# Kernel optimization log

Hardware: AMD Instinct MI355X
Metric: run time of the kernel (lower is better)

## Reference

```python
import jax, jax.numpy as jnp
import numpy as np

B, S, H, F, K = 32, 512, 256, 256, 3
NBINS, MAX_MEL = 256, 2048


def _conv1d(x, w, b):
    # x: [B,S,Cin], w: [K,Cin,Cout] -> [B,S,Cout], padding 1 (SAME, k=3)
    return jax.lax.conv_general_dilated(x, w, (1,), 'SAME',
        dimension_numbers=('NWC', 'WIO', 'NWC')) + b


def _ln(x, g, b):
    m = jnp.mean(x, -1, keepdims=True)
    v = jnp.var(x, -1, keepdims=True)
    return (x - m) * jax.lax.rsqrt(v + 1e-5) * g + b


def _predictor(x, mask, p):
    # FastSpeech2 VariancePredictor (eval mode, dropout off)
    w1, b1, g1, be1, w2, b2, g2, be2, wl, bl = p
    h = _ln(jax.nn.relu(_conv1d(x, w1, b1)), g1, be1)
    h = _ln(jax.nn.relu(_conv1d(h, w2, b2)), g2, be2)
    out = (h @ wl + bl)[..., 0]  # [B,S]
    return jnp.where(mask, 0.0, out)  # masked_fill(mask, 0.0)


def _make_predictor_params(key, out_bias):
    ks = jax.random.split(key, 3)
    w1 = jax.random.normal(ks[0], (K, H, F), jnp.float32) * 0.03
    w2 = jax.random.normal(ks[1], (K, F, F), jnp.float32) * 0.03
    wl = jax.random.normal(ks[2], (F, 1), jnp.float32) * 0.02
    return [w1, jnp.zeros((F,), jnp.float32), jnp.ones((F,), jnp.float32), jnp.zeros((F,), jnp.float32),
            w2, jnp.zeros((F,), jnp.float32), jnp.ones((F,), jnp.float32), jnp.zeros((F,), jnp.float32),
            wl, jnp.full((1,), out_bias, jnp.float32)]


PNAMES = ['w1', 'b1', 'g1', 'be1', 'w2', 'b2', 'g2', 'be2', 'wl', 'bl']


def setup_inputs() -> dict:
    key = jax.random.key(0)
    ks = jax.random.split(key, 8)
    inp = {
        'x': jax.random.normal(ks[0], (B, S, H), jnp.float32),
        'src_mask': jnp.zeros((B, S), jnp.bool_),  # True = padded position
        'pitch_control': jnp.float32(1.0),
        'energy_control': jnp.float32(1.0),
        'duration_control': jnp.float32(1.0),
        'pitch_bins': jnp.linspace(-4.0, 4.0, NBINS - 1, dtype=jnp.float32),
        'energy_bins': jnp.linspace(-4.0, 4.0, NBINS - 1, dtype=jnp.float32),
        'pitch_emb': jax.random.normal(ks[1], (NBINS, H), jnp.float32) * 0.02,
        'energy_emb': jax.random.normal(ks[2], (NBINS, H), jnp.float32) * 0.02,
    }
    # duration predictor output bias 1.6 ~ log(5) -> avg ~4 frames/phoneme
    for i, (pref, ob) in enumerate([('dur', 1.6), ('pit', 0.0), ('ene', 0.0)]):
        for n, v in zip(PNAMES, _make_predictor_params(ks[3 + i], ob)):
            inp[pref + '_' + n] = v
    return inp


def reference(x, src_mask, pitch_control, energy_control, duration_control,
              pitch_bins, energy_bins, pitch_emb, energy_emb,
              dur_w1, dur_b1, dur_g1, dur_be1, dur_w2, dur_b2, dur_g2, dur_be2, dur_wl, dur_bl,
              pit_w1, pit_b1, pit_g1, pit_be1, pit_w2, pit_b2, pit_g2, pit_be2, pit_wl, pit_bl,
              ene_w1, ene_b1, ene_g1, ene_be1, ene_w2, ene_b2, ene_g2, ene_be2, ene_wl, ene_bl):
    dur_p = [dur_w1, dur_b1, dur_g1, dur_be1, dur_w2, dur_b2, dur_g2, dur_be2, dur_wl, dur_bl]
    pit_p = [pit_w1, pit_b1, pit_g1, pit_be1, pit_w2, pit_b2, pit_g2, pit_be2, pit_wl, pit_bl]
    ene_p = [ene_w1, ene_b1, ene_g1, ene_be1, ene_w2, ene_b2, ene_g2, ene_be2, ene_wl, ene_bl]

    log_dur = _predictor(x, src_mask, dur_p)                      # [B,S]
    pitch_pred = _predictor(x, src_mask, pit_p) * pitch_control   # inference: scaled prediction
    # torch.bucketize(v, bins) (right=False) == searchsorted side='left'
    x = x + pitch_emb[jnp.searchsorted(pitch_bins, pitch_pred, side='left')]
    energy_pred = _predictor(x, src_mask, ene_p) * energy_control
    x = x + energy_emb[jnp.searchsorted(energy_bins, energy_pred, side='left')]

    dur = jnp.maximum(jnp.round(jnp.exp(log_dur) - 1.0) * duration_control, 0.0)  # [B,S]
    dur_i = dur.astype(jnp.int32)
    mel_len = jnp.minimum(jnp.sum(dur_i, -1), MAX_MEL)            # [B]
    # Length regulator: frame t maps to phoneme idx = #{cumdur <= t}
    cum = jnp.cumsum(dur_i, 1)                                    # [B,S]
    t = jnp.arange(MAX_MEL, dtype=jnp.int32)
    idx = jax.vmap(lambda c: jnp.searchsorted(c, t, side='right'))(cum)  # [B,MAX_MEL]
    idx = jnp.clip(idx, 0, S - 1)
    x_exp = jnp.take_along_axis(x, idx[:, :, None], axis=1)       # [B,MAX_MEL,H]
    mel_mask = t[None, :] >= mel_len[:, None]                     # True = padded frame
    x_exp = jnp.where(mel_mask[:, :, None], 0.0, x_exp)
    return (x_exp, pitch_pred, energy_pred, log_dur, dur, mel_len, mel_mask)
```

## Files before the change

kernel.cpp:

```cpp
#include <hip/hip_runtime.h>
#include <stdint.h>

#define BB 32
#define SS 512
#define HH 256
#define MM (BB*SS)
#define MAXMEL 2048

typedef _Float16 f16;
typedef _Float16 f16x4 __attribute__((ext_vector_type(4)));
typedef _Float16 f16x8 __attribute__((ext_vector_type(8)));
typedef float    f32x16 __attribute__((ext_vector_type(16)));

#define BAR()  asm volatile("s_barrier" ::: "memory")
#define VMW9() asm volatile("s_waitcnt vmcnt(9)" ::: "memory")
#define VMW0() asm volatile("s_waitcnt vmcnt(0)" ::: "memory")

__device__ __forceinline__ size_t xoff8(int pane, int row) {
  return ((size_t)pane * MM + row) * 8;
}

#define AOFF  49152
#define ABUF  12352
#define AZ    61440
#define BBUF  24576
#define LDSSZ 73856
#define WSZP ((size_t)393216)

template<int NS, int RAW>
__global__ __launch_bounds__(256) void conv16(
    const f16* __restrict__ X0h, const f16* __restrict__ X0l,
    const f16* __restrict__ X1h_, const f16* __restrict__ X1l_,
    const f16* __restrict__ W0, const f16* __restrict__ W1,
    const float* __restrict__ bias0, const float* __restrict__ bias1,
    f16* __restrict__ Y0h, f16* __restrict__ Y0l,
    f16* __restrict__ Y1h, f16* __restrict__ Y1l,
    float* __restrict__ Craw)
{
  __shared__ __align__(16) unsigned char smem[LDSSZ];
  const int tid = threadIdx.x;
  const int lane = tid & 63, wid = tid >> 6;
  const int bm = blockIdx.x, bn = blockIdx.y, bz = blockIdx.z;
  const int l31 = lane & 31, half = lane >> 5;
  const int wr = wid >> 1, wc = wid & 1;

  const int s0 = RAW ? bz * 8 : 0;
  const f16* Xh = (RAW || bz == 0) ? X0h : X1h_;
  const f16* Xl = (RAW || bz == 0) ? X0l : X1l_;
  const f16* Wp = (RAW || bz == 0) ? W0 : W1;

  const f16* sb[9]; int sdst[9]; int sdb[9]; size_t sstr[9];
  #pragma unroll
  for (int i = 0; i < 9; ++i) {
    int j = wid * 9 + i;
    if (j < 12) {
      int p = j / 6, rem = j % 6, g = rem / 3, seg = rem % 3;
      int lr = seg * 64 + lane;
      int row = bm * 128 - 32 + lr;
      row = row < 0 ? 0 : (row >= MM ? MM - 1 : row);
      sb[i]   = (p ? Xl : Xh) + ((size_t)g * MM + row) * 8;
      sstr[i] = (size_t)MM * 16;
      sdst[i] = AOFF + p * 6144 + g * 3072 + lr * 16;
      sdb[i]  = ABUF;
    } else {
      int jj = j - 12;
      int p = jj / 12, rest = jj % 12;
      int tap = rest >> 2, q = rest & 3;
      int g = q >> 1, h2 = q & 1;
      sb[i]   = Wp + ((((((size_t)(bn * 16) * 2 + p) * 3 + tap) * 2 + g) * 128)
                      + h2 * 64 + lane) * 8;
      sstr[i] = 12288;
      sdst[i] = p * 12288 + tap * 4096 + g * 2048 + h2 * 1024 + lane * 16;
      sdb[i]  = BBUF;
    }
  }

  int a_addr[3][2][2];
  #pragma unroll
  for (int tap = 0; tap < 3; ++tap)
    #pragma unroll
    for (int mi = 0; mi < 2; ++mi) {
      int row_l = wr * 64 + mi * 32 + l31;
      int sseq = (bm & 3) * 128 + row_l + tap - 1;
      bool valid = (unsigned)sseq < 512u;
      int lr = row_l + tap + 31;
      #pragma unroll
      for (int p = 0; p < 2; ++p)
        a_addr[tap][mi][p] = valid ? (AOFF + p * 6144 + half * 3072 + lr * 16)
                                   : AZ;
    }
  int b_base[2];
  #pragma unroll
  for (int n = 0; n < 2; ++n)
    b_base[n] = half * 2048 + (wc * 64 + n * 32 + l31) * 16;

  f32x16 acc[2][2];
  #pragma unroll
  for (int mi = 0; mi < 2; ++mi)
    #pragma unroll
    for (int ni = 0; ni < 2; ++ni) acc[mi][ni] = (f32x16)0.f;

  auto STAGE = [&](int buf, int step) {
    #pragma unroll
    for (int i = 0; i < 9; ++i)
      __builtin_amdgcn_global_load_lds(
        (const __attribute__((address_space(1))) void*)(sb[i] + (size_t)step * sstr[i]),
        (__attribute__((address_space(3))) void*)(smem + sdst[i] + buf * sdb[i]),
        16, 0, 0);
  };

  auto COMP = [&](int buf) {
    #pragma unroll
    for (int tap = 0; tap < 3; ++tap) {
      f16x8 av[2][2], bv[2][2];
      #pragma unroll
      for (int p = 0; p < 2; ++p)
        #pragma unroll
        for (int q = 0; q < 2; ++q) {
          av[p][q] = *(const f16x8*)(smem + (a_addr[tap][q][p] + buf * ABUF));
          bv[p][q] = *(const f16x8*)(smem + (buf * BBUF + p * 12288 + tap * 4096 + b_base[q]));
        }
      #pragma unroll
      for (int mi = 0; mi < 2; ++mi)
        #pragma unroll
        for (int ni = 0; ni < 2; ++ni) {
          acc[mi][ni] = __builtin_amdgcn_mfma_f32_32x32x16_f16(av[0][mi], bv[0][ni], acc[mi][ni], 0, 0, 0);
          acc[mi][ni] = __builtin_amdgcn_mfma_f32_32x32x16_f16(av[0][mi], bv[1][ni], acc[mi][ni], 0, 0, 0);
          acc[mi][ni] = __builtin_amdgcn_mfma_f32_32x32x16_f16(av[1][mi], bv[0][ni], acc[mi][ni], 0, 0, 0);
        }
    }
  };

  if (tid < 4) {
    *(float4*)(smem + AZ + tid * 16) = make_float4(0.f, 0.f, 0.f, 0.f);
    *(float4*)(smem + AZ + ABUF + tid * 16) = make_float4(0.f, 0.f, 0.f, 0.f);
  }
  STAGE(0, s0); STAGE(1, s0 + 1);
  __syncthreads();

  #pragma unroll
  for (int i = 0; i < NS; ++i) {
    COMP(i & 1);
    BAR();
    if (i < NS - 2)       { STAGE(i & 1, s0 + i + 2); VMW9(); }
    else if (i == NS - 2) { VMW0(); }
    BAR();
  }

  if constexpr (RAW) {
    float* C = Craw + (size_t)bz * MM * 256;
    #pragma unroll
    for (int mi = 0; mi < 2; ++mi)
      #pragma unroll
      for (int ni = 0; ni < 2; ++ni) {
        int colg = bn * 128 + wc * 64 + ni * 32 + l31;
        #pragma unroll
        for (int r = 0; r < 16; ++r) {
          int rowl = (r & 3) + 8 * (r >> 2) + 4 * half;
          size_t rowg = (size_t)bm * 128 + wr * 64 + mi * 32 + rowl;
          C[rowg * 256 + colg] = acc[mi][ni][r];
        }
      }
  } else {
    const float* bias = bz ? bias1 : bias0;
    f16* Yh = bz ? Y1h : Y0h;
    f16* Yl = bz ? Y1l : Y0l;
    #pragma unroll
    for (int mi = 0; mi < 2; ++mi)
      #pragma unroll
      for (int ni = 0; ni < 2; ++ni) {
        int colg = bn * 128 + wc * 64 + ni * 32 + l31;
        float bvs = bias[colg];
        size_t cbase = (size_t)(colg >> 3) * MM * 8 + (colg & 7);
        #pragma unroll
        for (int r = 0; r < 16; ++r) {
          int rowl = (r & 3) + 8 * (r >> 2) + 4 * half;
          int rowg = bm * 128 + wr * 64 + mi * 32 + rowl;
          float v = fmaxf(acc[mi][ni][r] + bvs, 0.f);
          f16 h = (f16)v;
          f16 l = (f16)(v - (float)h);
          size_t o = cbase + (size_t)rowg * 8;
          Yh[o] = h;
          Yl[o] = l;
        }
      }
  }
}

__global__ __launch_bounds__(256) void wsplit6(
    const float* __restrict__ W0, const float* __restrict__ W1,
    const float* __restrict__ W2, const float* __restrict__ W3,
    const float* __restrict__ W4, const float* __restrict__ W5,
    f16* __restrict__ Wt)
{
  int z = blockIdx.y;
  const float* W = z==0?W0 : z==1?W1 : z==2?W2 : z==3?W3 : z==4?W4 : W5;
  f16* T = Wt + (size_t)z * WSZP;
  int id = blockIdx.x * 256 + threadIdx.x;
  int col = id & 127;
  int t = id >> 7;
  int g = t & 1; t >>= 1;
  int tap = t % 3; t /= 3;
  int p = t & 1; t >>= 1;
  int s = t & 15;
  int bn = t >> 4;
  int chan = s * 16 + g * 8;
  int colg = bn * 128 + col;
  f16x8 o;
  #pragma unroll
  for (int e = 0; e < 8; ++e) {
    float w = W[(size_t)(tap * 256 + chan + e) * 256 + colg];
    f16 h = (f16)w;
    o[e] = p ? (f16)(w - (float)h) : h;
  }
  *(f16x8*)(T + (size_t)id * 8) = o;
}

__global__ __launch_bounds__(256) void split2(
    const float* __restrict__ X, f16* __restrict__ Hi, f16* __restrict__ Lo)
{
  int id = blockIdx.x * 256 + threadIdx.x;
  int row = id >> 5, pane = id & 31;
  const float* src = X + (size_t)row * 256 + pane * 8;
  float4 v0 = *(const float4*)src;
  float4 v1 = *(const float4*)(src + 4);
  float vv[8] = {v0.x, v0.y, v0.z, v0.w, v1.x, v1.y, v1.z, v1.w};
  f16x8 h, l;
  #pragma unroll
  for (int j = 0; j < 8; ++j) {
    f16 hh = (f16)vv[j];
    h[j] = hh;
    l[j] = (f16)(vv[j] - (float)hh);
  }
  size_t o = xoff8(pane, row);
  *(f16x8*)(Hi + o) = h;
  *(f16x8*)(Lo + o) = l;
}


__global__ __launch_bounds__(256) void lnF(
    f16* __restrict__ P0h, f16* __restrict__ P0l,
    f16* __restrict__ P1h, f16* __restrict__ P1l,
    const float* __restrict__ g0, const float* __restrict__ be0,
    const float* __restrict__ g1, const float* __restrict__ be1)
{
  int z = blockIdx.y;
  f16* Ph = z ? P1h : P0h;
  f16* Pl = z ? P1l : P0l;
  const float* g  = z ? g1 : g0;
  const float* be = z ? be1 : be0;
  int tid = threadIdx.x, lane = tid & 63;
  int row  = blockIdx.x * 8 + (tid >> 6) * 2 + (lane >> 5);
  int pane = lane & 31;
  size_t o = xoff8(pane, row);
  f16x8 h = *(const f16x8*)(Ph + o);
  f16x8 l = *(const f16x8*)(Pl + o);
  float v[8];
  #pragma unroll
  for (int j = 0; j < 8; ++j) v[j] = (float)h[j] + (float)l[j];
  float s = 0.f, q = 0.f;
  #pragma unroll
  for (int j = 0; j < 8; ++j) { s += v[j]; q += v[j] * v[j]; }
  #pragma unroll
  for (int d = 16; d > 0; d >>= 1) { s += __shfl_xor(s, d); q += __shfl_xor(q, d); }
  float mean = s * (1.f / 256.f);
  float var  = q * (1.f / 256.f) - mean * mean;
  float inv  = 1.0f / sqrtf(var + 1e-5f);
  float4 ga = *(const float4*)(g + pane * 8);
  float4 gb = *(const float4*)(g + pane * 8 + 4);
  float4 ba = *(const float4*)(be + pane * 8);
  float4 bb = *(const float4*)(be + pane * 8 + 4);
  float gv[8] = {ga.x, ga.y, ga.z, ga.w, gb.x, gb.y, gb.z, gb.w};
  float bv[8] = {ba.x, ba.y, ba.z, ba.w, bb.x, bb.y, bb.z, bb.w};
  #pragma unroll
  for (int j = 0; j < 8; ++j) {
    float oo = (v[j] - mean) * inv * gv[j] + bv[j];
    f16 hh = (f16)oo;
    h[j] = hh;
    l[j] = (f16)(oo - (float)hh);
  }
  *(f16x8*)(Ph + o) = h;
  *(f16x8*)(Pl + o) = l;
}

__global__ __launch_bounds__(256) void lnheadD(
    const f16* __restrict__ U0h, const f16* __restrict__ U0l,
    const f16* __restrict__ U1h, const f16* __restrict__ U1l,
    const float* __restrict__ g0, const float* __restrict__ be0,
    const float* __restrict__ wl0, const float* __restrict__ bl0,
    const float* __restrict__ g1, const float* __restrict__ be1,
    const float* __restrict__ wl1, const float* __restrict__ bl1,
    const unsigned char* __restrict__ mask, const float* __restrict__ pc,
    float* __restrict__ o_ldur, float* __restrict__ pred_d,
    float* __restrict__ o_pit,
    const float* __restrict__ pbins, const float* __restrict__ pemb,
    const f16* __restrict__ XPh, const f16* __restrict__ XPl,
    f16* __restrict__ X1h, f16* __restrict__ X1l)
{
  int z = blockIdx.y;
  int tid = threadIdx.x, lane = tid & 63;
  int row  = blockIdx.x * 8 + (tid >> 6) * 2 + (lane >> 5);
  int pane = lane & 31;
  size_t o = xoff8(pane, row);
  const f16* Uh = z ? U1h : U0h;
  const f16* Ul = z ? U1l : U0l;
  f16x8 h = *(const f16x8*)(Uh + o);
  f16x8 l = *(const f16x8*)(Ul + o);
  float v[8];
  #pragma unroll
  for (int j = 0; j < 8; ++j) v[j] = (float)h[j] + (float)l[j];
  float s = 0.f, q = 0.f;
  #pragma unroll
  for (int j = 0; j < 8; ++j) { s += v[j]; q += v[j] * v[j]; }
  #pragma unroll
  for (int d = 16; d > 0; d >>= 1) { s += __shfl_xor(s, d); q += __shfl_xor(q, d); }
  float mean = s * (1.f / 256.f);
  float var  = q * (1.f / 256.f) - mean * mean;
  float inv  = 1.0f / sqrtf(var + 1e-5f);
  const float* g  = z ? g1  : g0;
  const float* be = z ? be1 : be0;
  const float* wl = z ? wl1 : wl0;
  float4 ga = *(const float4*)(g + pane * 8);
  float4 gb = *(const float4*)(g + pane * 8 + 4);
  float4 ba = *(const float4*)(be + pane * 8);
  float4 bb = *(const float4*)(be + pane * 8 + 4);
  float4 wa = *(const float4*)(wl + pane * 8);
  float4 wb = *(const float4*)(wl + pane * 8 + 4);
  float gv[8] = {ga.x, ga.y, ga.z, ga.w, gb.x, gb.y, gb.z, gb.w};
  float bv[8] = {ba.x, ba.y, ba.z, ba.w, bb.x, bb.y, bb.z, bb.w};
  float wv[8] = {wa.x, wa.y, wa.z, wa.w, wb.x, wb.y, wb.z, wb.w};
  float acc = 0.f;
  #pragma unroll
  for (int j = 0; j < 8; ++j)
    acc += ((v[j] - mean) * inv * gv[j] + bv[j]) * wv[j];
  #pragma unroll
  for (int d = 16; d > 0; d >>= 1) acc += __shfl_xor(acc, d);
  float r = acc + (z ? bl1 : bl0)[0];
  if (mask[row]) r = 0.f;
  if (z == 0) {
    if (pane == 0) { o_ldur[row] = r; pred_d[row] = r; }
  } else {
    r *= pc[0];
    if (pane == 0) o_pit[row] = r;
    int lo = 0, hi = 255;
    while (lo < hi) { int mid = (lo + hi) >> 1; if (pbins[mid] < r) lo = mid + 1; else hi = mid; }
    f16x8 xh = *(const f16x8*)(XPh + o);
    f16x8 xl = *(const f16x8*)(XPl + o);
    float4 ea = *(const float4*)(pemb + (size_t)lo * HH + pane * 8);
    float4 eb = *(const float4*)(pemb + (size_t)lo * HH + pane * 8 + 4);
    float ev[8] = {ea.x, ea.y, ea.z, ea.w, eb.x, eb.y, eb.z, eb.w};
    #pragma unroll
    for (int j = 0; j < 8; ++j) {
      float oo = (float)xh[j] + (float)xl[j] + ev[j];
      f16 hh = (f16)oo;
      xh[j] = hh;
      xl[j] = (f16)(oo - (float)hh);
    }
    *(f16x8*)(X1h + o) = xh;
    *(f16x8*)(X1l + o) = xl;
  }
}

__global__ __launch_bounds__(256) void lnS(
    const float* __restrict__ C0, const float* __restrict__ C1,
    const float* __restrict__ bias,
    const float* __restrict__ g, const float* __restrict__ be,
    f16* __restrict__ Yh, f16* __restrict__ Yl)
{
  int tid = threadIdx.x, lane = tid & 63;
  int row  = blockIdx.x * 8 + (tid >> 6) * 2 + (lane >> 5);
  int pane = lane & 31;
  size_t ci = (size_t)row * 256 + pane * 8;
  float4 a0 = *(const float4*)(C0 + ci);
  float4 a1 = *(const float4*)(C0 + ci + 4);
  float4 b0 = *(const float4*)(C1 + ci);
  float4 b1 = *(const float4*)(C1 + ci + 4);
  float4 s0 = *(const float4*)(bias + pane * 8);
  float4 s1 = *(const float4*)(bias + pane * 8 + 4);
  float v[8] = {fmaxf(a0.x + b0.x + s0.x, 0.f), fmaxf(a0.y + b0.y + s0.y, 0.f),
                fmaxf(a0.z + b0.z + s0.z, 0.f), fmaxf(a0.w + b0.w + s0.w, 0.f),
                fmaxf(a1.x + b1.x + s1.x, 0.f), fmaxf(a1.y + b1.y + s1.y, 0.f),
                fmaxf(a1.z + b1.z + s1.z, 0.f), fmaxf(a1.w + b1.w + s1.w, 0.f)};
  float s = 0.f, q = 0.f;
  #pragma unroll
  for (int j = 0; j < 8; ++j) { s += v[j]; q += v[j] * v[j]; }
  #pragma unroll
  for (int d = 16; d > 0; d >>= 1) { s += __shfl_xor(s, d); q += __shfl_xor(q, d); }
  float mean = s * (1.f / 256.f);
  float var  = q * (1.f / 256.f) - mean * mean;
  float inv  = 1.0f / sqrtf(var + 1e-5f);
  float4 ga = *(const float4*)(g + pane * 8);
  float4 gb = *(const float4*)(g + pane * 8 + 4);
  float4 ba = *(const float4*)(be + pane * 8);
  float4 bb = *(const float4*)(be + pane * 8 + 4);
  float gv[8] = {ga.x, ga.y, ga.z, ga.w, gb.x, gb.y, gb.z, gb.w};
  float bv[8] = {ba.x, ba.y, ba.z, ba.w, bb.x, bb.y, bb.z, bb.w};
  f16x8 h, l;
  #pragma unroll
  for (int j = 0; j < 8; ++j) {
    float oo = (v[j] - mean) * inv * gv[j] + bv[j];
    f16 hh = (f16)oo;
    h[j] = hh;
    l[j] = (f16)(oo - (float)hh);
  }
  size_t o = xoff8(pane, row);
  *(f16x8*)(Yh + o) = h;
  *(f16x8*)(Yl + o) = l;
}

__global__ __launch_bounds__(256) void lnheadS(
    const float* __restrict__ C0, const float* __restrict__ C1,
    const float* __restrict__ bias,
    const float* __restrict__ g, const float* __restrict__ be,
    const float* __restrict__ wl, const float* __restrict__ bl,
    const unsigned char* __restrict__ mask, const float* __restrict__ ec,
    float* __restrict__ o_ene,
    const float* __restrict__ ebins, const float* __restrict__ eemb,
    const f16* __restrict__ X1h, const f16* __restrict__ X1l,
    f16* __restrict__ X2h, f16* __restrict__ X2l)
{
  int tid = threadIdx.x, lane = tid & 63;
  int row  = blockIdx.x * 8 + (tid >> 6) * 2 + (lane >> 5);
  int pane = lane & 31;
  size_t ci = (size_t)row * 256 + pane * 8;
  float4 a0 = *(const float4*)(C0 + ci);
  float4 a1 = *(const float4*)(C0 + ci + 4);
  float4 b0 = *(const float4*)(C1 + ci);
  float4 b1 = *(const float4*)(C1 + ci + 4);
  float4 s0 = *(const float4*)(bias + pane * 8);
  float4 s1 = *(const float4*)(bias + pane * 8 + 4);
  float v[8] = {fmaxf(a0.x + b0.x + s0.x, 0.f), fmaxf(a0.y + b0.y + s0.y, 0.f),
                fmaxf(a0.z + b0.z + s0.z, 0.f), fmaxf(a0.w + b0.w + s0.w, 0.f),
                fmaxf(a1.x + b1.x + s1.x, 0.f), fmaxf(a1.y + b1.y + s1.y, 0.f),
                fmaxf(a1.z + b1.z + s1.z, 0.f), fmaxf(a1.w + b1.w + s1.w, 0.f)};
  float s = 0.f, q = 0.f;
  #pragma unroll
  for (int j = 0; j < 8; ++j) { s += v[j]; q += v[j] * v[j]; }
  #pragma unroll
  for (int d = 16; d > 0; d >>= 1) { s += __shfl_xor(s, d); q += __shfl_xor(q, d); }
  float mean = s * (1.f / 256.f);
  float var  = q * (1.f / 256.f) - mean * mean;
  float inv  = 1.0f / sqrtf(var + 1e-5f);
  float4 ga = *(const float4*)(g + pane * 8);
  float4 gb = *(const float4*)(g + pane * 8 + 4);
  float4 ba = *(const float4*)(be + pane * 8);
  float4 bb = *(const float4*)(be + pane * 8 + 4);
  float4 wa = *(const float4*)(wl + pane * 8);
  float4 wb = *(const float4*)(wl + pane * 8 + 4);
  float gv[8] = {ga.x, ga.y, ga.z, ga.w, gb.x, gb.y, gb.z, gb.w};
  float bv[8] = {ba.x, ba.y, ba.z, ba.w, bb.x, bb.y, bb.z, bb.w};
  float wv[8] = {wa.x, wa.y, wa.z, wa.w, wb.x, wb.y, wb.z, wb.w};
  float acc = 0.f;
  #pragma unroll
  for (int j = 0; j < 8; ++j)
    acc += ((v[j] - mean) * inv * gv[j] + bv[j]) * wv[j];
  #pragma unroll
  for (int d = 16; d > 0; d >>= 1) acc += __shfl_xor(acc, d);
  float r = acc + bl[0];
  if (mask[row]) r = 0.f;
  r *= ec[0];
  if (pane == 0) o_ene[row] = r;
  int lo = 0, hi = 255;
  while (lo < hi) { int mid = (lo + hi) >> 1; if (ebins[mid] < r) lo = mid + 1; else hi = mid; }
  size_t o = xoff8(pane, row);
  f16x8 xh = *(const f16x8*)(X1h + o);
  f16x8 xl = *(const f16x8*)(X1l + o);
  float4 ea = *(const float4*)(eemb + (size_t)lo * HH + pane * 8);
  float4 eb = *(const float4*)(eemb + (size_t)lo * HH + pane * 8 + 4);
  float ev[8] = {ea.x, ea.y, ea.z, ea.w, eb.x, eb.y, eb.z, eb.w};
  #pragma unroll
  for (int j = 0; j < 8; ++j) {
    float oo = (float)xh[j] + (float)xl[j] + ev[j];
    f16 hh = (f16)oo;
    xh[j] = hh;
    xl[j] = (f16)(oo - (float)hh);
  }
  *(f16x8*)(X2h + o) = xh;
  *(f16x8*)(X2l + o) = xl;
}

__global__ __launch_bounds__(512) void dur_post(
    const float* __restrict__ logdur, const float* __restrict__ dc,
    float* __restrict__ out_dur, float* __restrict__ out_mel_len,
    int* __restrict__ cum_ws, int* __restrict__ mel_len_ws)
{
  __shared__ int wsum[8];
  int b = blockIdx.x, t = threadIdx.x;
  float ld = logdur[b * SS + t];
  float d  = fmaxf(rintf(expf(ld) - 1.f) * dc[0], 0.f);
  out_dur[b * SS + t] = d;
  int di = (int)d;
  int lane = t & 63, w = t >> 6;
  int x = di;
  #pragma unroll
  for (int dd = 1; dd < 64; dd <<= 1) {
    int n = __shfl_up(x, dd);
    if (lane >= dd) x += n;
  }
  if (lane == 63) wsum[w] = x;
  __syncthreads();
  int off = 0;
  for (int i = 0; i < w; ++i) off += wsum[i];
  x += off;
  cum_ws[b * SS + t] = x;
  if (t == SS - 1) {
    int ml = min(x, MAXMEL);
    mel_len_ws[b] = ml;
    out_mel_len[b] = (float)ml;
  }
}

__global__ __launch_bounds__(256) void gather_planes(
    const f16* __restrict__ Xhi, const f16* __restrict__ Xlo,
    const int* __restrict__ cum, const int* __restrict__ mel_len_ws,
    float* __restrict__ out_x, float* __restrict__ out_mask)
{
  __shared__ int c[SS];
  int b   = blockIdx.y;
  int tid = threadIdx.x;
  c[tid]       = cum[b * SS + tid];
  c[tid + 256] = cum[b * SS + tid + 256];
  __syncthreads();
  int lane = tid & 63, w = tid >> 6;
  int t = blockIdx.x * 8 + w * 2 + (lane >> 5);
  int pane = lane & 31;
  int lo = 0, hi = SS;
  while (lo < hi) { int mid = (lo + hi) >> 1; if (c[mid] <= t) lo = mid + 1; else hi = mid; }
  int idx = min(lo, SS - 1);
  int ml  = mel_len_ws[b];
  bool m  = (t >= ml);
  float v[8] = {0.f, 0.f, 0.f, 0.f, 0.f, 0.f, 0.f, 0.f};
  if (!m) {
    size_t o = xoff8(pane, b * SS + idx);
    f16x8 xh = *(const f16x8*)(Xhi + o);
    f16x8 xl = *(const f16x8*)(Xlo + o);
    #pragma unroll
    for (int j = 0; j < 8; ++j) v[j] = (float)xh[j] + (float)xl[j];
  }
  float* dst = out_x + ((size_t)b * MAXMEL + t) * HH + pane * 8;
  *(float4*)dst       = make_float4(v[0], v[1], v[2], v[3]);
  *(float4*)(dst + 4) = make_float4(v[4], v[5], v[6], v[7]);
  if (pane == 0) out_mask[b * MAXMEL + t] = m ? 1.f : 0.f;
}

extern "C" void kernel_launch(void* const* d_in, const int* in_sizes, int n_in,
                              void* d_out, int out_size, void* d_ws, size_t ws_size,
                              hipStream_t stream) {
  const float* x     = (const float*)d_in[0];
  const unsigned char* smask = (const unsigned char*)d_in[1];
  const float* pc    = (const float*)d_in[2];
  const float* ec    = (const float*)d_in[3];
  const float* dc    = (const float*)d_in[4];
  const float* pbins = (const float*)d_in[5];
  const float* ebins = (const float*)d_in[6];
  const float* pemb  = (const float*)d_in[7];
  const float* eemb  = (const float*)d_in[8];

  float* out = (float*)d_out;
  float* o_xexp  = out;
  float* o_pit   = out + (size_t)16777216;
  float* o_ene   = o_pit + 16384;
  float* o_ldur  = o_ene + 16384;
  float* o_dur   = o_ldur + 16384;
  float* o_mlen  = o_dur + 16384;
  float* o_mmask = o_mlen + 32;

  const size_t PL = (size_t)MM * HH;
  f16* p = (f16*)d_ws;
  f16 *XPh = p,        *XPl = p + PL;
  f16 *Tdh = p + 2*PL, *Tdl = p + 3*PL;
  f16 *Tph = p + 4*PL, *Tpl = p + 5*PL;
  f16 *Udh = p + 6*PL, *Udl = p + 7*PL;
  f16 *Uph = p + 8*PL, *Upl = p + 9*PL;
  f16 *X1h = p + 10*PL, *X1l = p + 11*PL;
  f16 *Teh = p + 12*PL, *Tel = p + 13*PL;
  f16 *X2h = p + 14*PL, *X2l = p + 15*PL;
  f16* Wt  = p + 16*PL;
  float* C0 = (float*)(Wt + 6 * WSZP);
  float* C1 = C0 + (size_t)MM * 256;
  float* pred_d = C1 + (size_t)MM * 256;
  int*   cum = (int*)(pred_d + MM);
  int*   mlw = cum + MM;

  #define WPK(i) (Wt + (size_t)(i) * WSZP)

  wsplit6<<<dim3(192, 6), 256, 0, stream>>>(
      (const float*)d_in[9], (const float*)d_in[13], (const float*)d_in[19],
      (const float*)d_in[23], (const float*)d_in[29], (const float*)d_in[33], Wt);

  split2<<<2048, 256, 0, stream>>>(x, XPh, XPl);

  dim3 cgrid(128, 2, 2);
  dim3 rgrid8(MM / 8);
  dim3 rgrid8x2(MM / 8, 2);

  conv16<16, 0><<<cgrid, 256, 0, stream>>>(
      XPh, XPl, XPh, XPl, WPK(0), WPK(2),
      (const float*)d_in[10], (const float*)d_in[20],
      Tdh, Tdl, Tph, Tpl, nullptr);
  lnF<<<rgrid8x2, 256, 0, stream>>>(Tdh, Tdl, Tph, Tpl,
      (const float*)d_in[11], (const float*)d_in[12],
      (const float*)d_in[21], (const float*)d_in[22]);
  conv16<16, 0><<<cgrid, 256, 0, stream>>>(
      Tdh, Tdl, Tph, Tpl, WPK(1), WPK(3),
      (const float*)d_in[14], (const float*)d_in[24],
      Udh, Udl, Uph, Upl, nullptr);
  lnheadD<<<rgrid8x2, 256, 0, stream>>>(
      Udh, Udl, Uph, Upl,
      (const float*)d_in[15], (const float*)d_in[16],
      (const float*)d_in[17], (const float*)d_in[18],
      (const float*)d_in[25], (const float*)d_in[26],
      (const float*)d_in[27], (const float*)d_in[28],
      smask, pc, o_ldur, pred_d, o_pit, pbins, pemb,
      XPh, XPl, X1h, X1l);
  dur_post<<<BB, 512, 0, stream>>>(pred_d, dc, o_dur, o_mlen, cum, mlw);

  conv16<8, 1><<<cgrid, 256, 0, stream>>>(
      X1h, X1l, X1h, X1l, WPK(4), WPK(4),
      nullptr, nullptr, nullptr, nullptr, nullptr, nullptr, C0);
  lnS<<<rgrid8, 256, 0, stream>>>(C0, C1, (const float*)d_in[30],
      (const float*)d_in[31], (const float*)d_in[32], Teh, Tel);
  conv16<8, 1><<<cgrid, 256, 0, stream>>>(
      Teh, Tel, Teh, Tel, WPK(5), WPK(5),
      nullptr, nullptr, nullptr, nullptr, nullptr, nullptr, C0);
  lnheadS<<<rgrid8, 256, 0, stream>>>(C0, C1, (const float*)d_in[34],
      (const float*)d_in[35], (const float*)d_in[36],
      (const float*)d_in[37], (const float*)d_in[38],
      smask, ec, o_ene, ebins, eemb, X1h, X1l, X2h, X2l);

  dim3 ggrid(MAXMEL / 8, BB);
  gather_planes<<<ggrid, 256, 0, stream>>>(X2h, X2l, cum, mlw, o_xexp, o_mmask);

  #undef WPK
}
```

Baseline: 233.0 us.

## Fuse LayerNorm and predictor head into full-width conv epilogue

The duration and pitch conv kernels now compute all 256 output channels per block (512 threads, 8 waves), so the LayerNorm row statistics and the linear head can be computed in the conv epilogue through LDS reductions. This removes the separate lnF and lnheadD kernels and their round trips of the intermediate fp16 hi/lo planes through global memory. The weight packing layout changes to a full-width format, and the energy split-K conv is adapted to read it. The trade-off is half as many blocks with a larger LDS footprint, which lowers occupancy and parallelism.

```diff
diff --git a/kernel.cpp b/kernel.cpp
--- a/kernel.cpp
+++ b/kernel.cpp
@@ -14,40 +14,296 @@
 
 #define BAR()  asm volatile("s_barrier" ::: "memory")
 #define VMW9() asm volatile("s_waitcnt vmcnt(9)" ::: "memory")
+#define VMW8() asm volatile("s_waitcnt vmcnt(8)" ::: "memory")
+#define VMW7() asm volatile("s_waitcnt vmcnt(7)" ::: "memory")
 #define VMW0() asm volatile("s_waitcnt vmcnt(0)" ::: "memory")
 
 __device__ __forceinline__ size_t xoff8(int pane, int row) {
   return ((size_t)pane * MM + row) * 8;
 }
 
-#define AOFF  49152
-#define ABUF  12352
-#define AZ    61440
-#define BBUF  24576
-#define LDSSZ 73856
 #define WSZP ((size_t)393216)
 
-template<int NS, int RAW>
-__global__ __launch_bounds__(256) void conv16(
+#define CBSTR 49152
+#define CAOFF 98304
+#define CABUF 12352
+#define CAZ   110592
+#define CLDS  123008
+#define PSOFF 0
+#define MNOFF 4096
+#define DPOFF 5120
+#define BKOFF 7168
+
+template<int MODE>
+__global__ __launch_bounds__(512) void conv256(
     const f16* __restrict__ X0h, const f16* __restrict__ X0l,
     const f16* __restrict__ X1h_, const f16* __restrict__ X1l_,
     const f16* __restrict__ W0, const f16* __restrict__ W1,
     const float* __restrict__ bias0, const float* __restrict__ bias1,
+    const float* __restrict__ g0, const float* __restrict__ be0,
+    const float* __restrict__ g1, const float* __restrict__ be1,
     f16* __restrict__ Y0h, f16* __restrict__ Y0l,
     f16* __restrict__ Y1h, f16* __restrict__ Y1l,
+    const float* __restrict__ wl0, const float* __restrict__ bl0,
+    const float* __restrict__ wl1, const float* __restrict__ bl1,
+    const unsigned char* __restrict__ mask, const float* __restrict__ pc,
+    float* __restrict__ o_ldur, float* __restrict__ pred_d,
+    float* __restrict__ o_pit,
+    const float* __restrict__ pbins, const float* __restrict__ pemb,
+    const f16* __restrict__ XPh, const f16* __restrict__ XPl,
+    f16* __restrict__ XO1h, f16* __restrict__ XO1l)
+{
+  __shared__ __align__(16) unsigned char smem[CLDS];
+  const int tid = threadIdx.x;
+  const int lane = tid & 63, wid = tid >> 6;
+  const int bm = blockIdx.x, bz = blockIdx.z;
+  const int l31 = lane & 31, half = lane >> 5;
+  const int wr = wid >> 2, wc = wid & 3;
+
+  const f16* Xh = bz ? X1h_ : X0h;
+  const f16* Xl = bz ? X1l_ : X0l;
+  const f16* Wp = bz ? W1 : W0;
+
+  const f16* sb[8]; int sdst[8]; int sdb[8]; size_t sstr[8];
+  #pragma unroll
+  for (int i = 0; i < 8; ++i) {
+    int j = (wid < 4) ? (wid * 8 + i) : (32 + (wid - 4) * 7 + i);
+    if (j > 59) j = 32;
+    if (j < 12) {
+      int p = j / 6, rem = j % 6, g = rem / 3, seg = rem % 3;
+      int lr = seg * 64 + lane;
+      int row = bm * 128 - 32 + lr;
+      row = row < 0 ? 0 : (row >= MM ? MM - 1 : row);
+      sb[i]   = (p ? Xl : Xh) + ((size_t)g * MM + row) * 8;
+      sstr[i] = (size_t)MM * 16;
+      sdst[i] = CAOFF + p * 6144 + g * 3072 + lr * 16;
+      sdb[i]  = CABUF;
+    } else {
+      int jj = j - 12;
+      int p = jj / 24, rest = jj % 24;
+      int tap = rest >> 3, rem = rest & 7;
+      int g = rem >> 2, q4 = rem & 3;
+      sb[i]   = Wp + ((((size_t)(p * 3 + tap) * 2 + g) * 256) + q4 * 64 + lane) * 8;
+      sstr[i] = 24576;
+      sdst[i] = p * 24576 + tap * 8192 + g * 4096 + q4 * 1024 + lane * 16;
+      sdb[i]  = CBSTR;
+    }
+  }
+
+  int a_addr[3][2][2];
+  #pragma unroll
+  for (int tap = 0; tap < 3; ++tap)
+    #pragma unroll
+    for (int mi = 0; mi < 2; ++mi) {
+      int row_l = wr * 64 + mi * 32 + l31;
+      int sseq = (bm & 3) * 128 + row_l + tap - 1;
+      bool valid = (unsigned)sseq < 512u;
+      int lr = row_l + tap + 31;
+      #pragma unroll
+      for (int p = 0; p < 2; ++p)
+        a_addr[tap][mi][p] = valid ? (CAOFF + p * 6144 + half * 3072 + lr * 16)
+                                   : CAZ;
+    }
+  int b_base[2];
+  #pragma unroll
+  for (int n = 0; n < 2; ++n)
+    b_base[n] = half * 4096 + (wc * 64 + n * 32 + l31) * 16;
+
+  f32x16 acc[2][2];
+  #pragma unroll
+  for (int mi = 0; mi < 2; ++mi)
+    #pragma unroll
+    for (int ni = 0; ni < 2; ++ni) acc[mi][ni] = (f32x16)0.f;
+
+  auto STAGE = [&](int buf, int step) {
+    #pragma unroll
+    for (int i = 0; i < 7; ++i)
+      __builtin_amdgcn_global_load_lds(
+        (const __attribute__((address_space(1))) void*)(sb[i] + (size_t)step * sstr[i]),
+        (__attribute__((address_space(3))) void*)(smem + sdst[i] + buf * sdb[i]),
+        16, 0, 0);
+    if (wid < 4)
+      __builtin_amdgcn_global_load_lds(
+        (const __attribute__((address_space(1))) void*)(sb[7] + (size_t)step * sstr[7]),
+        (__attribute__((address_space(3))) void*)(smem + sdst[7] + buf * sdb[7]),
+        16, 0, 0);
+  };
+
+  auto COMP = [&](int buf) {
+    #pragma unroll
+    for (int tap = 0; tap < 3; ++tap) {
+      f16x8 av[2][2], bv[2][2];
+      #pragma unroll
+      for (int p = 0; p < 2; ++p)
+        #pragma unroll
+        for (int q = 0; q < 2; ++q) {
+          av[p][q] = *(const f16x8*)(smem + (a_addr[tap][q][p] + buf * CABUF));
+          bv[p][q] = *(const f16x8*)(smem + (buf * CBSTR + p * 24576 + tap * 8192 + b_base[q]));
+        }
+      #pragma unroll
+      for (int mi = 0; mi < 2; ++mi)
+        #pragma unroll
+        for (int ni = 0; ni < 2; ++ni) {
+          acc[mi][ni] = __builtin_amdgcn_mfma_f32_32x32x16_f16(av[0][mi], bv[0][ni], acc[mi][ni], 0, 0, 0);
+          acc[mi][ni] = __builtin_amdgcn_mfma_f32_32x32x16_f16(av[0][mi], bv[1][ni], acc[mi][ni], 0, 0, 0);
+          acc[mi][ni] = __builtin_amdgcn_mfma_f32_32x32x16_f16(av[1][mi], bv[0][ni], acc[mi][ni], 0, 0, 0);
+        }
+    }
+  };
+
+  if (tid < 4) {
+    *(float4*)(smem + CAZ + tid * 16) = make_float4(0.f, 0.f, 0.f, 0.f);
+    *(float4*)(smem + CAZ + CABUF + tid * 16) = make_float4(0.f, 0.f, 0.f, 0.f);
+  }
+  STAGE(0, 0); STAGE(1, 1);
+  __syncthreads();
+
+  #pragma unroll
+  for (int i = 0; i < 16; ++i) {
+    COMP(i & 1);
+    BAR();
+    if (i < 14)       { STAGE(i & 1, i + 2); if (wid < 4) VMW8(); else VMW7(); }
+    else if (i == 14) { VMW0(); }
+    BAR();
+  }
+
+  const float* bias = bz ? bias1 : bias0;
+  const float* gam  = bz ? g1 : g0;
+  const float* bet  = bz ? be1 : be0;
+  const int colg0 = wc * 64 + l31;
+  const int colg1 = colg0 + 32;
+  const float bq0 = bias[colg0], bq1 = bias[colg1];
+
+  #pragma unroll
+  for (int mi = 0; mi < 2; ++mi)
+    #pragma unroll
+    for (int r = 0; r < 16; ++r) {
+      float v0 = fmaxf(acc[mi][0][r] + bq0, 0.f);
+      float v1 = fmaxf(acc[mi][1][r] + bq1, 0.f);
+      float s = v0 + v1, q = v0 * v0 + v1 * v1;
+      #pragma unroll
+      for (int d = 16; d > 0; d >>= 1) { s += __shfl_xor(s, d); q += __shfl_xor(q, d); }
+      if (l31 == 0) {
+        int row_l = wr * 64 + mi * 32 + (r & 3) + 8 * (r >> 2) + 4 * half;
+        *(float2*)(smem + PSOFF + (row_l * 4 + wc) * 8) = make_float2(s, q);
+      }
+    }
+  BAR();
+  if (tid < 128) {
+    int row = tid;
+    float s = 0.f, q = 0.f;
+    #pragma unroll
+    for (int w = 0; w < 4; ++w) {
+      float2 pq = *(float2*)(smem + PSOFF + (row * 4 + w) * 8);
+      s += pq.x; q += pq.y;
+    }
+    float mean = s * (1.f / 256.f);
+    float var  = q * (1.f / 256.f) - mean * mean;
+    float inv  = 1.0f / sqrtf(var + 1e-5f);
+    *(float2*)(smem + MNOFF + row * 8) = make_float2(mean, inv);
+  }
+  BAR();
+
+  const float gv0 = gam[colg0], gv1 = gam[colg1];
+  const float bv0 = bet[colg0], bv1 = bet[colg1];
+  size_t cb0 = (size_t)(colg0 >> 3) * MM * 8 + (colg0 & 7);
+  size_t cb1 = (size_t)(colg1 >> 3) * MM * 8 + (colg1 & 7);
+
+  if constexpr (MODE == 0) {
+    f16* Yh = bz ? Y1h : Y0h;
+    f16* Yl = bz ? Y1l : Y0l;
+    #pragma unroll
+    for (int mi = 0; mi < 2; ++mi)
+      #pragma unroll
+      for (int r = 0; r < 16; ++r) {
+        int row_l = wr * 64 + mi * 32 + (r & 3) + 8 * (r >> 2) + 4 * half;
+        int rowg = bm * 128 + row_l;
+        float2 m2 = *(float2*)(smem + MNOFF + row_l * 8);
+        float v0 = fmaxf(acc[mi][0][r] + bq0, 0.f);
+        float v1 = fmaxf(acc[mi][1][r] + bq1, 0.f);
+        float o0 = (v0 - m2.x) * m2.y * gv0 + bv0;
+        float o1 = (v1 - m2.x) * m2.y * gv1 + bv1;
+        f16 h0 = (f16)o0, h1 = (f16)o1;
+        size_t p0 = cb0 + (size_t)rowg * 8, p1 = cb1 + (size_t)rowg * 8;
+        Yh[p0] = h0; Yl[p0] = (f16)(o0 - (float)h0);
+        Yh[p1] = h1; Yl[p1] = (f16)(o1 - (float)h1);
+      }
+  } else {
+    const float* wl = bz ? wl1 : wl0;
+    const float wv0 = wl[colg0], wv1 = wl[colg1];
+    #pragma unroll
+    for (int mi = 0; mi < 2; ++mi)
+      #pragma unroll
+      for (int r = 0; r < 16; ++r) {
+        int row_l = wr * 64 + mi * 32 + (r & 3) + 8 * (r >> 2) + 4 * half;
+        float2 m2 = *(float2*)(smem + MNOFF + row_l * 8);
+        float v0 = fmaxf(acc[mi][0][r] + bq0, 0.f);
+        float v1 = fmaxf(acc[mi][1][r] + bq1, 0.f);
+        float dp = ((v0 - m2.x) * m2.y * gv0 + bv0) * wv0
+                 + ((v1 - m2.x) * m2.y * gv1 + bv1) * wv1;
+        #pragma unroll
+        for (int d = 16; d > 0; d >>= 1) dp += __shfl_xor(dp, d);
+        if (l31 == 0)
+          *(float*)(smem + DPOFF + (row_l * 4 + wc) * 4) = dp;
+      }
+    BAR();
+    if (tid < 128) {
+      int row = tid, rowg = bm * 128 + row;
+      float hd = (bz ? bl1 : bl0)[0];
+      #pragma unroll
+      for (int w = 0; w < 4; ++w) hd += *(float*)(smem + DPOFF + (row * 4 + w) * 4);
+      if (mask[rowg]) hd = 0.f;
+      if (bz == 0) {
+        o_ldur[rowg] = hd;
+        pred_d[rowg] = hd;
+      } else {
+        hd *= pc[0];
+        o_pit[rowg] = hd;
+        int lo = 0, hi = 255;
+        while (lo < hi) { int mid = (lo + hi) >> 1; if (pbins[mid] < hd) lo = mid + 1; else hi = mid; }
+        *(int*)(smem + BKOFF + row * 4) = lo;
+      }
+    }
+    if (bz == 1) {
+      BAR();
+      #pragma unroll
+      for (int mi = 0; mi < 2; ++mi)
+        #pragma unroll
+        for (int r = 0; r < 16; ++r) {
+          int row_l = wr * 64 + mi * 32 + (r & 3) + 8 * (r >> 2) + 4 * half;
+          int rowg = bm * 128 + row_l;
+          int bkt = *(int*)(smem + BKOFF + row_l * 4);
+          float e0 = pemb[(size_t)bkt * HH + colg0];
+          float e1 = pemb[(size_t)bkt * HH + colg1];
+          size_t p0 = cb0 + (size_t)rowg * 8, p1 = cb1 + (size_t)rowg * 8;
+          float x0 = (float)XPh[p0] + (float)XPl[p0] + e0;
+          float x1 = (float)XPh[p1] + (float)XPl[p1] + e1;
+          f16 h0 = (f16)x0, h1 = (f16)x1;
+          XO1h[p0] = h0; XO1l[p0] = (f16)(x0 - (float)h0);
+          XO1h[p1] = h1; XO1l[p1] = (f16)(x1 - (float)h1);
+        }
+    }
+  }
+}
+
+#define KAOFF  49152
+#define KABUF  12352
+#define KAZ    61440
+#define KBBUF  24576
+#define KLDS   73856
+
+__global__ __launch_bounds__(256) void convKS(
+    const f16* __restrict__ Xh, const f16* __restrict__ Xl,
+    const f16* __restrict__ Wp,
     float* __restrict__ Craw)
 {
-  __shared__ __align__(16) unsigned char smem[LDSSZ];
+  __shared__ __align__(16) unsigned char smem[KLDS];
   const int tid = threadIdx.x;
   const int lane = tid & 63, wid = tid >> 6;
   const int bm = blockIdx.x, bn = blockIdx.y, bz = blockIdx.z;
   const int l31 = lane & 31, half = lane >> 5;
   const int wr = wid >> 1, wc = wid & 1;
-
-  const int s0 = RAW ? bz * 8 : 0;
-  const f16* Xh = (RAW || bz == 0) ? X0h : X1h_;
-  const f16* Xl = (RAW || bz == 0) ? X0l : X1l_;
-  const f16* Wp = (RAW || bz == 0) ? W0 : W1;
+  const int s0 = bz * 8;
 
   const f16* sb[9]; int sdst[9]; int sdb[9]; size_t sstr[9];
   #pragma unroll
@@ -60,18 +316,17 @@
       row = row < 0 ? 0 : (row >= MM ? MM - 1 : row);
       sb[i]   = (p ? Xl : Xh) + ((size_t)g * MM + row) * 8;
       sstr[i] = (size_t)MM * 16;
-      sdst[i] = AOFF + p * 6144 + g * 3072 + lr * 16;
-      sdb[i]  = ABUF;
+      sdst[i] = KAOFF + p * 6144 + g * 3072 + lr * 16;
+      sdb[i]  = KABUF;
     } else {
       int jj = j - 12;
       int p = jj / 12, rest = jj % 12;
       int tap = rest >> 2, q = rest & 3;
       int g = q >> 1, h2 = q & 1;
-      sb[i]   = Wp + ((((((size_t)(bn * 16) * 2 + p) * 3 + tap) * 2 + g) * 128)
-                      + h2 * 64 + lane) * 8;
-      sstr[i] = 12288;
+      sb[i]   = Wp + ((((size_t)(p * 3 + tap) * 2 + g) * 256) + bn * 128 + h2 * 64 + lane) * 8;
+      sstr[i] = 24576;
       sdst[i] = p * 12288 + tap * 4096 + g * 2048 + h2 * 1024 + lane * 16;
-      sdb[i]  = BBUF;
+      sdb[i]  = KBBUF;
     }
   }
 
@@ -86,8 +341,7 @@
       int lr = row_l + tap + 31;
       #pragma unroll
       for (int p = 0; p < 2; ++p)
-        a_addr[tap][mi][p] = valid ? (AOFF + p * 6144 + half * 3072 + lr * 16)
-                                   : AZ;
+        a_addr[tap][mi][p] = valid ? (KAOFF + p * 6144 + half * 3072 + lr * 16) : KAZ;
     }
   int b_base[2];
   #pragma unroll
@@ -117,8 +371,8 @@
       for (int p = 0; p < 2; ++p)
         #pragma unroll
         for (int q = 0; q < 2; ++q) {
-          av[p][q] = *(const f16x8*)(smem + (a_addr[tap][q][p] + buf * ABUF));
-          bv[p][q] = *(const f16x8*)(smem + (buf * BBUF + p * 12288 + tap * 4096 + b_base[q]));
+          av[p][q] = *(const f16x8*)(smem + (a_addr[tap][q][p] + buf * KABUF));
+          bv[p][q] = *(const f16x8*)(smem + (buf * KBBUF + p * 12288 + tap * 4096 + b_base[q]));
         }
       #pragma unroll
       for (int mi = 0; mi < 2; ++mi)
@@ -132,59 +386,34 @@
   };
 
   if (tid < 4) {
-    *(float4*)(smem + AZ + tid * 16) = make_float4(0.f, 0.f, 0.f, 0.f);
-    *(float4*)(smem + AZ + ABUF + tid * 16) = make_float4(0.f, 0.f, 0.f, 0.f);
+    *(float4*)(smem + KAZ + tid * 16) = make_float4(0.f, 0.f, 0.f, 0.f);
+    *(float4*)(smem + KAZ + KABUF + tid * 16) = make_float4(0.f, 0.f, 0.f, 0.f);
   }
   STAGE(0, s0); STAGE(1, s0 + 1);
   __syncthreads();
 
   #pragma unroll
-  for (int i = 0; i < NS; ++i) {
+  for (int i = 0; i < 8; ++i) {
     COMP(i & 1);
     BAR();
-    if (i < NS - 2)       { STAGE(i & 1, s0 + i + 2); VMW9(); }
-    else if (i == NS - 2) { VMW0(); }
+    if (i < 6)       { STAGE(i & 1, s0 + i + 2); VMW9(); }
+    else if (i == 6) { VMW0(); }
     BAR();
   }
 
-  if constexpr (RAW) {
-    float* C = Craw + (size_t)bz * MM * 256;
-    #pragma unroll
-    for (int mi = 0; mi < 2; ++mi)
-      #pragma unroll
-      for (int ni = 0; ni < 2; ++ni) {
-        int colg = bn * 128 + wc * 64 + ni * 32 + l31;
-        #pragma unroll
-        for (int r = 0; r < 16; ++r) {
-          int rowl = (r & 3) + 8 * (r >> 2) + 4 * half;
-          size_t rowg = (size_t)bm * 128 + wr * 64 + mi * 32 + rowl;
-          C[rowg * 256 + colg] = acc[mi][ni][r];
-        }
+  float* C = Craw + (size_t)bz * MM * 256;
+  #pragma unroll
+  for (int mi = 0; mi < 2; ++mi)
+    #pragma unroll
+    for (int ni = 0; ni < 2; ++ni) {
+      int colg = bn * 128 + wc * 64 + ni * 32 + l31;
+      #pragma unroll
+      for (int r = 0; r < 16; ++r) {
+        int rowl = (r & 3) + 8 * (r >> 2) + 4 * half;
+        size_t rowg = (size_t)bm * 128 + wr * 64 + mi * 32 + rowl;
+        C[rowg * 256 + colg] = acc[mi][ni][r];
       }
-  } else {
-    const float* bias = bz ? bias1 : bias0;
-    f16* Yh = bz ? Y1h : Y0h;
-    f16* Yl = bz ? Y1l : Y0l;
-    #pragma unroll
-    for (int mi = 0; mi < 2; ++mi)
-      #pragma unroll
-      for (int ni = 0; ni < 2; ++ni) {
-        int colg = bn * 128 + wc * 64 + ni * 32 + l31;
-        float bvs = bias[colg];
-        size_t cbase = (size_t)(colg >> 3) * MM * 8 + (colg & 7);
-        #pragma unroll
-        for (int r = 0; r < 16; ++r) {
-          int rowl = (r & 3) + 8 * (r >> 2) + 4 * half;
-          int rowg = bm * 128 + wr * 64 + mi * 32 + rowl;
-          float v = fmaxf(acc[mi][ni][r] + bvs, 0.f);
-          f16 h = (f16)v;
-          f16 l = (f16)(v - (float)h);
-          size_t o = cbase + (size_t)rowg * 8;
-          Yh[o] = h;
-          Yl[o] = l;
-        }
-      }
-  }
+    }
 }
 
 __global__ __launch_bounds__(256) void wsplit6(
@@ -197,19 +426,17 @@
   const float* W = z==0?W0 : z==1?W1 : z==2?W2 : z==3?W3 : z==4?W4 : W5;
   f16* T = Wt + (size_t)z * WSZP;
   int id = blockIdx.x * 256 + threadIdx.x;
-  int col = id & 127;
-  int t = id >> 7;
+  int col = id & 255;
+  int t = id >> 8;
   int g = t & 1; t >>= 1;
   int tap = t % 3; t /= 3;
   int p = t & 1; t >>= 1;
-  int s = t & 15;
-  int bn = t >> 4;
+  int s = t;
   int chan = s * 16 + g * 8;
-  int colg = bn * 128 + col;
   f16x8 o;
   #pragma unroll
   for (int e = 0; e < 8; ++e) {
-    float w = W[(size_t)(tap * 256 + chan + e) * 256 + colg];
+    float w = W[(size_t)(tap * 256 + chan + e) * 256 + col];
     f16 h = (f16)w;
     o[e] = p ? (f16)(w - (float)h) : h;
   }
@@ -235,130 +462,6 @@
   size_t o = xoff8(pane, row);
   *(f16x8*)(Hi + o) = h;
   *(f16x8*)(Lo + o) = l;
-}
-
-
-__global__ __launch_bounds__(256) void lnF(
-    f16* __restrict__ P0h, f16* __restrict__ P0l,
-    f16* __restrict__ P1h, f16* __restrict__ P1l,
-    const float* __restrict__ g0, const float* __restrict__ be0,
-    const float* __restrict__ g1, const float* __restrict__ be1)
-{
-  int z = blockIdx.y;
-  f16* Ph = z ? P1h : P0h;
-  f16* Pl = z ? P1l : P0l;
-  const float* g  = z ? g1 : g0;
-  const float* be = z ? be1 : be0;
-  int tid = threadIdx.x, lane = tid & 63;
-  int row  = blockIdx.x * 8 + (tid >> 6) * 2 + (lane >> 5);
-  int pane = lane & 31;
-  size_t o = xoff8(pane, row);
-  f16x8 h = *(const f16x8*)(Ph + o);
-  f16x8 l = *(const f16x8*)(Pl + o);
-  float v[8];
-  #pragma unroll
-  for (int j = 0; j < 8; ++j) v[j] = (float)h[j] + (float)l[j];
-  float s = 0.f, q = 0.f;
-  #pragma unroll
-  for (int j = 0; j < 8; ++j) { s += v[j]; q += v[j] * v[j]; }
-  #pragma unroll
-  for (int d = 16; d > 0; d >>= 1) { s += __shfl_xor(s, d); q += __shfl_xor(q, d); }
-  float mean = s * (1.f / 256.f);
-  float var  = q * (1.f / 256.f) - mean * mean;
-  float inv  = 1.0f / sqrtf(var + 1e-5f);
-  float4 ga = *(const float4*)(g + pane * 8);
-  float4 gb = *(const float4*)(g + pane * 8 + 4);
-  float4 ba = *(const float4*)(be + pane * 8);
-  float4 bb = *(const float4*)(be + pane * 8 + 4);
-  float gv[8] = {ga.x, ga.y, ga.z, ga.w, gb.x, gb.y, gb.z, gb.w};
-  float bv[8] = {ba.x, ba.y, ba.z, ba.w, bb.x, bb.y, bb.z, bb.w};
-  #pragma unroll
-  for (int j = 0; j < 8; ++j) {
-    float oo = (v[j] - mean) * inv * gv[j] + bv[j];
-    f16 hh = (f16)oo;
-    h[j] = hh;
-    l[j] = (f16)(oo - (float)hh);
-  }
-  *(f16x8*)(Ph + o) = h;
-  *(f16x8*)(Pl + o) = l;
-}
-
-__global__ __launch_bounds__(256) void lnheadD(
-    const f16* __restrict__ U0h, const f16* __restrict__ U0l,
-    const f16* __restrict__ U1h, const f16* __restrict__ U1l,
-    const float* __restrict__ g0, const float* __restrict__ be0,
-    const float* __restrict__ wl0, const float* __restrict__ bl0,
-    const float* __restrict__ g1, const float* __restrict__ be1,
-    const float* __restrict__ wl1, const float* __restrict__ bl1,
-    const unsigned char* __restrict__ mask, const float* __restrict__ pc,
-    float* __restrict__ o_ldur, float* __restrict__ pred_d,
-    float* __restrict__ o_pit,
-    const float* __restrict__ pbins, const float* __restrict__ pemb,
-    const f16* __restrict__ XPh, const f16* __restrict__ XPl,
-    f16* __restrict__ X1h, f16* __restrict__ X1l)
-{
-  int z = blockIdx.y;
-  int tid = threadIdx.x, lane = tid & 63;
-  int row  = blockIdx.x * 8 + (tid >> 6) * 2 + (lane >> 5);
-  int pane = lane & 31;
-  size_t o = xoff8(pane, row);
-  const f16* Uh = z ? U1h : U0h;
-  const f16* Ul = z ? U1l : U0l;
-  f16x8 h = *(const f16x8*)(Uh + o);
-  f16x8 l = *(const f16x8*)(Ul + o);
-  float v[8];
-  #pragma unroll
-  for (int j = 0; j < 8; ++j) v[j] = (float)h[j] + (float)l[j];
-  float s = 0.f, q = 0.f;
-  #pragma unroll
-  for (int j = 0; j < 8; ++j) { s += v[j]; q += v[j] * v[j]; }
-  #pragma unroll
-  for (int d = 16; d > 0; d >>= 1) { s += __shfl_xor(s, d); q += __shfl_xor(q, d); }
-  float mean = s * (1.f / 256.f);
-  float var  = q * (1.f / 256.f) - mean * mean;
-  float inv  = 1.0f / sqrtf(var + 1e-5f);
-  const float* g  = z ? g1  : g0;
-  const float* be = z ? be1 : be0;
-  const float* wl = z ? wl1 : wl0;
-  float4 ga = *(const float4*)(g + pane * 8);
-  float4 gb = *(const float4*)(g + pane * 8 + 4);
-  float4 ba = *(const float4*)(be + pane * 8);
-  float4 bb = *(const float4*)(be + pane * 8 + 4);
-  float4 wa = *(const float4*)(wl + pane * 8);
-  float4 wb = *(const float4*)(wl + pane * 8 + 4);
-  float gv[8] = {ga.x, ga.y, ga.z, ga.w, gb.x, gb.y, gb.z, gb.w};
-  float bv[8] = {ba.x, ba.y, ba.z, ba.w, bb.x, bb.y, bb.z, bb.w};
-  float wv[8] = {wa.x, wa.y, wa.z, wa.w, wb.x, wb.y, wb.z, wb.w};
-  float acc = 0.f;
-  #pragma unroll
-  for (int j = 0; j < 8; ++j)
-    acc += ((v[j] - mean) * inv * gv[j] + bv[j]) * wv[j];
-  #pragma unroll
-  for (int d = 16; d > 0; d >>= 1) acc += __shfl_xor(acc, d);
-  float r = acc + (z ? bl1 : bl0)[0];
-  if (mask[row]) r = 0.f;
-  if (z == 0) {
-    if (pane == 0) { o_ldur[row] = r; pred_d[row] = r; }
-  } else {
-    r *= pc[0];
-    if (pane == 0) o_pit[row] = r;
-    int lo = 0, hi = 255;
-    while (lo < hi) { int mid = (lo + hi) >> 1; if (pbins[mid] < r) lo = mid + 1; else hi = mid; }
-    f16x8 xh = *(const f16x8*)(XPh + o);
-    f16x8 xl = *(const f16x8*)(XPl + o);
-    float4 ea = *(const float4*)(pemb + (size_t)lo * HH + pane * 8);
-    float4 eb = *(const float4*)(pemb + (size_t)lo * HH + pane * 8 + 4);
-    float ev[8] = {ea.x, ea.y, ea.z, ea.w, eb.x, eb.y, eb.z, eb.w};
-    #pragma unroll
-    for (int j = 0; j < 8; ++j) {
-      float oo = (float)xh[j] + (float)xl[j] + ev[j];
-      f16 hh = (f16)oo;
-      xh[j] = hh;
-      xl[j] = (f16)(oo - (float)hh);
-    }
-    *(f16x8*)(X1h + o) = xh;
-    *(f16x8*)(X1l + o) = xl;
-  }
 }
 
 __global__ __launch_bounds__(256) void lnS(
@@ -570,12 +673,10 @@
   f16 *XPh = p,        *XPl = p + PL;
   f16 *Tdh = p + 2*PL, *Tdl = p + 3*PL;
   f16 *Tph = p + 4*PL, *Tpl = p + 5*PL;
-  f16 *Udh = p + 6*PL, *Udl = p + 7*PL;
-  f16 *Uph = p + 8*PL, *Upl = p + 9*PL;
-  f16 *X1h = p + 10*PL, *X1l = p + 11*PL;
-  f16 *Teh = p + 12*PL, *Tel = p + 13*PL;
-  f16 *X2h = p + 14*PL, *X2l = p + 15*PL;
-  f16* Wt  = p + 16*PL;
+  f16 *X1h = p + 6*PL, *X1l = p + 7*PL;
+  f16 *Teh = p + 8*PL, *Tel = p + 9*PL;
+  f16 *X2h = p + 10*PL, *X2l = p + 11*PL;
+  f16* Wt  = p + 12*PL;
   float* C0 = (float*)(Wt + 6 * WSZP);
   float* C1 = C0 + (size_t)MM * 256;
   float* pred_d = C1 + (size_t)MM * 256;
@@ -590,39 +691,35 @@
 
   split2<<<2048, 256, 0, stream>>>(x, XPh, XPl);
 
-  dim3 cgrid(128, 2, 2);
+  dim3 cgrid256(128, 1, 2);
+  dim3 kgrid(128, 2, 2);
   dim3 rgrid8(MM / 8);
-  dim3 rgrid8x2(MM / 8, 2);
-
-  conv16<16, 0><<<cgrid, 256, 0, stream>>>(
+
+  conv256<0><<<cgrid256, 512, 0, stream>>>(
       XPh, XPl, XPh, XPl, WPK(0), WPK(2),
       (const float*)d_in[10], (const float*)d_in[20],
-      Tdh, Tdl, Tph, Tpl, nullptr);
-  lnF<<<rgrid8x2, 256, 0, stream>>>(Tdh, Tdl, Tph, Tpl,
       (const float*)d_in[11], (const float*)d_in[12],
-      (const float*)d_in[21], (const float*)d_in[22]);
-  conv16<16, 0><<<cgrid, 256, 0, stream>>>(
+      (const float*)d_in[21], (const float*)d_in[22],
+      Tdh, Tdl, Tph, Tpl,
+      nullptr, nullptr, nullptr, nullptr,
+      nullptr, nullptr, nullptr, nullptr, nullptr,
+      nullptr, nullptr, nullptr, nullptr, nullptr, nullptr);
+  conv256<1><<<cgrid256, 512, 0, stream>>>(
       Tdh, Tdl, Tph, Tpl, WPK(1), WPK(3),
       (const float*)d_in[14], (const float*)d_in[24],
-      Udh, Udl, Uph, Upl, nullptr);
-  lnheadD<<<rgrid8x2, 256, 0, stream>>>(
-      Udh, Udl, Uph, Upl,
       (const float*)d_in[15], (const float*)d_in[16],
+      (const float*)d_in[25], (const float*)d_in[26],
+      nullptr, nullptr, nullptr, nullptr,
       (const float*)d_in[17], (const float*)d_in[18],
-      (const float*)d_in[25], (const float*)d_in[26],
       (const float*)d_in[27], (const float*)d_in[28],
       smask, pc, o_ldur, pred_d, o_pit, pbins, pemb,
       XPh, XPl, X1h, X1l);
   dur_post<<<BB, 512, 0, stream>>>(pred_d, dc, o_dur, o_mlen, cum, mlw);
 
-  conv16<8, 1><<<cgrid, 256, 0, stream>>>(
-      X1h, X1l, X1h, X1l, WPK(4), WPK(4),
-      nullptr, nullptr, nullptr, nullptr, nullptr, nullptr, C0);
+  convKS<<<kgrid, 256, 0, stream>>>(X1h, X1l, WPK(4), C0);
   lnS<<<rgrid8, 256, 0, stream>>>(C0, C1, (const float*)d_in[30],
       (const float*)d_in[31], (const float*)d_in[32], Teh, Tel);
-  conv16<8, 1><<<cgrid, 256, 0, stream>>>(
-      Teh, Tel, Teh, Tel, WPK(5), WPK(5),
-      nullptr, nullptr, nullptr, nullptr, nullptr, nullptr, C0);
+  convKS<<<kgrid, 256, 0, stream>>>(Teh, Tel, WPK(5), C0);
   lnheadS<<<rgrid8, 256, 0, stream>>>(C0, C1, (const float*)d_in[34],
       (const float*)d_in[35], (const float*)d_in[36],
       (const float*)d_in[37], (const float*)d_in[38],
```

Result: no change. 228.5 us (-1.9%).
